# Optimization experiments

Hardware: AMD Instinct MI355X
Metric: run time of the kernel (lower is better)

The kernel has to match this reference:

```python
import jax, jax.numpy as jnp
import numpy as np

DIM = 384
NUM_HEADS = 8
HEAD_DIM = DIM // NUM_HEADS
SCALE = HEAD_DIM ** -0.5
MLP_HIDDEN = int(DIM * 4.0)
EPS = 1e-6


def setup_inputs() -> dict:
    key = jax.random.key(0)
    ks = jax.random.split(key, 8)
    s = 0.02
    return {
        "x": jax.random.normal(ks[0], (2, DIM, 8, 16, 16), dtype=jnp.float32),
        "g1": jnp.ones((DIM,), jnp.float32),
        "b1": jnp.zeros((DIM,), jnp.float32),
        "Wqkv": jax.random.normal(ks[1], (DIM, 3 * DIM), jnp.float32) * s,  # no bias (qkv_bias=False)
        "Wo": jax.random.normal(ks[2], (DIM, DIM), jnp.float32) * s,
        "bo": jnp.zeros((DIM,), jnp.float32),
        "g2": jnp.ones((DIM,), jnp.float32),
        "b2": jnp.zeros((DIM,), jnp.float32),
        "W1": jax.random.normal(ks[3], (DIM, MLP_HIDDEN), jnp.float32) * s,
        "b1m": jnp.zeros((MLP_HIDDEN,), jnp.float32),
        "W2": jax.random.normal(ks[4], (MLP_HIDDEN, DIM), jnp.float32) * s,
        "b2m": jnp.zeros((DIM,), jnp.float32),
    }


def _layernorm(x, g, b):
    mu = jnp.mean(x, axis=-1, keepdims=True)
    var = jnp.mean(jnp.square(x - mu), axis=-1, keepdims=True)
    return (x - mu) * jax.lax.rsqrt(var + EPS) * g + b


def _attention(h, Wqkv, Wo, bo):
    B, N, C = h.shape
    qkv = h @ Wqkv  # [B, N, 3C]
    qkv = qkv.reshape(B, N, 3, NUM_HEADS, HEAD_DIM).transpose(2, 0, 3, 1, 4)
    q, k, v = qkv[0], qkv[1], qkv[2]  # each [B, H, N, d]
    att = jax.nn.softmax(jnp.einsum('bhxd,bhyd->bhxy', q, k) * SCALE, axis=-1)
    out = jnp.einsum('bhxy,bhyd->bhxd', att, v)  # [B, H, N, d]
    out = out.transpose(0, 2, 1, 3).reshape(B, N, C)
    return out @ Wo + bo


def reference(x, g1, b1, Wqkv, Wo, bo, g2, b2, W1, b1m, W2, b2m):
    B, C, D, H, W = x.shape
    h = x.transpose(0, 2, 3, 4, 1).reshape(B, D * H * W, C)  # b (d h w) c
    h = h + _attention(_layernorm(h, g1, b1), Wqkv, Wo, bo)
    m = _layernorm(h, g2, b2)
    m = jax.nn.gelu(m @ W1 + b1m, approximate=False) @ W2 + b2m
    h = h + m
    return h.reshape(B, D, H, W, C).transpose(0, 4, 1, 2, 3)
```

## Files before the change

### kernel.cpp

```cpp
#include <hip/hip_runtime.h>
#include <hip/hip_bf16.h>
#include <math.h>

#define DIM    384
#define NHEAD  8
#define HDIM   48
#define NTOK   2048
#define BATCH  2
#define TOKS   (BATCH * NTOK)
#define HIDDEN 1536

typedef __bf16 bf16x8 __attribute__((ext_vector_type(8)));
typedef float  f32x4  __attribute__((ext_vector_type(4)));
typedef unsigned short u16;

union bfu { __hip_bfloat16 h; u16 u; };

__device__ __forceinline__ void load_lds16(const void* g, void* l) {
    __builtin_amdgcn_global_load_lds(
        (const __attribute__((address_space(1))) void*)g,
        (__attribute__((address_space(3))) void*)l, 16, 0, 0);
}

__global__ __launch_bounds__(256) void prep(
    const float* __restrict__ Wqkv, const float* __restrict__ Wo,
    const float* __restrict__ W1,   const float* __restrict__ W2,
    __hip_bfloat16* __restrict__ WqkvT, __hip_bfloat16* __restrict__ WoT,
    __hip_bfloat16* __restrict__ W1T,   __hip_bfloat16* __restrict__ W2T,
    const float* __restrict__ x, const float* __restrict__ g,
    const float* __restrict__ bta,
    float* __restrict__ hOut, __hip_bfloat16* __restrict__ y) {
    __shared__ __align__(16) char smem[384 * 33 * 4];
    int id = blockIdx.x;
    int tid = threadIdx.x;
    if (id < 1728) {
        float (*t)[33] = (float(*)[33])smem;
        const float* src; __hip_bfloat16* dst; int R, C;
        if (id < 432)       { src = Wqkv; dst = WqkvT; R = 384;  C = 1152; }
        else if (id < 576)  { id -= 432;  src = Wo;    dst = WoT;  R = 384;  C = 384; }
        else if (id < 1152) { id -= 576;  src = W1;    dst = W1T;  R = 384;  C = 1536; }
        else                { id -= 1152; src = W2;    dst = W2T;  R = 1536; C = 384; }
        int tc = C / 32;
        int i0 = (id / tc) * 32, j0 = (id % tc) * 32;
        int tx = tid & 31, ty = tid >> 5;
#pragma unroll
        for (int k = 0; k < 32; k += 8)
            t[ty + k][tx] = src[(size_t)(i0 + ty + k) * C + j0 + tx];
        __syncthreads();
#pragma unroll
        for (int k = 0; k < 32; k += 8)
            dst[(size_t)(j0 + ty + k) * R + i0 + tx] = __float2bfloat16(t[tx][ty + k]);
    } else {
        float* t = (float*)smem;
        int id2 = id - 1728;
        int n0 = (id2 & 63) * 32, b = id2 >> 6;
        const float* xb = x + (size_t)b * DIM * NTOK;
        for (int idx = tid; idx < 384 * 32; idx += 256) {
            int c = idx >> 5, n = idx & 31;
            t[c * 33 + n] = xb[(size_t)c * NTOK + n0 + n];
        }
        __syncthreads();
        int wid = tid >> 6, lane = tid & 63;
#pragma unroll
        for (int it = 0; it < 8; ++it) {
            int tl = it * 4 + wid;
            float v[6];
            float s = 0.f;
#pragma unroll
            for (int i = 0; i < 6; ++i) { v[i] = t[(lane + 64 * i) * 33 + tl]; s += v[i]; }
#pragma unroll
            for (int o = 32; o; o >>= 1) s += __shfl_xor(s, o, 64);
            float mu = s * (1.f / DIM);
            float s2 = 0.f;
#pragma unroll
            for (int i = 0; i < 6; ++i) { float d = v[i] - mu; s2 += d * d; }
#pragma unroll
            for (int o = 32; o; o >>= 1) s2 += __shfl_xor(s2, o, 64);
            float r = rsqrtf(s2 * (1.f / DIM) + 1e-6f);
            size_t tok = (size_t)b * NTOK + n0 + tl;
#pragma unroll
            for (int i = 0; i < 6; ++i) {
                int c = lane + 64 * i;
                hOut[tok * DIM + c] = v[i];
                y[tok * DIM + c] = __float2bfloat16((v[i] - mu) * r * g[c] + bta[c]);
            }
        }
    }
}

template<int BK, bool GELU, bool BF16OUT, bool TRANSOUT, bool QKV>
__global__ __launch_bounds__(256) void gemm_mfma(
    const __hip_bfloat16* __restrict__ A,
    const __hip_bfloat16* __restrict__ BT,
    const float* __restrict__ bias,
    const float* __restrict__ res,
    void* __restrict__ Cout,
    int M, int N, int K,
    __hip_bfloat16* __restrict__ vtout) {
    constexpr int NC = BK / 32;
    __shared__ __align__(16) u16 As[NC][64 * 32];
    __shared__ __align__(16) u16 Bs[NC][64 * 32];
    const int nwg = gridDim.x * gridDim.y;
    const int lid = blockIdx.y * gridDim.x + blockIdx.x;
    const int swz = (lid & 7) * (nwg >> 3) + (lid >> 3);
    const int bx = swz % gridDim.x, by = swz / gridDim.x;
    int bm = by * 64, bn = bx * 64;
    int tid = threadIdx.x;
    int w = tid >> 6, l = tid & 63;
    int m0 = (w >> 1) * 32, n0 = (w & 1) * 32;
    int lm = l & 15, ksel = l >> 4;

    int row = tid >> 2, c16 = tid & 3;
    const __hip_bfloat16* ga = A  + (size_t)(bm + row) * K + c16 * 8;
    const __hip_bfloat16* gb = BT + (size_t)(bn + row) * K + c16 * 8;

    f32x4 acc[2][2] = {};
    for (int k0 = 0; k0 < K; k0 += BK) {
#pragma unroll
        for (int c = 0; c < NC; ++c) {
            load_lds16(ga + k0 + c * 32, &As[c][tid * 8]);
            load_lds16(gb + k0 + c * 32, &Bs[c][tid * 8]);
        }
        __syncthreads();
#pragma unroll
        for (int kk = 0; kk < NC; ++kk) {
            bf16x8 af0 = *(const bf16x8*)&As[kk][(m0 +      lm) * 32 + ksel * 8];
            bf16x8 af1 = *(const bf16x8*)&As[kk][(m0 + 16 + lm) * 32 + ksel * 8];
            bf16x8 bf0 = *(const bf16x8*)&Bs[kk][(n0 +      lm) * 32 + ksel * 8];
            bf16x8 bf1 = *(const bf16x8*)&Bs[kk][(n0 + 16 + lm) * 32 + ksel * 8];
            acc[0][0] = __builtin_amdgcn_mfma_f32_16x16x32_bf16(af0, bf0, acc[0][0], 0, 0, 0);
            acc[0][1] = __builtin_amdgcn_mfma_f32_16x16x32_bf16(af0, bf1, acc[0][1], 0, 0, 0);
            acc[1][0] = __builtin_amdgcn_mfma_f32_16x16x32_bf16(af1, bf0, acc[1][0], 0, 0, 0);
            acc[1][1] = __builtin_amdgcn_mfma_f32_16x16x32_bf16(af1, bf1, acc[1][1], 0, 0, 0);
        }
        __syncthreads();
    }

    if constexpr (TRANSOUT) {
        __shared__ float ct[64 * 65];
#pragma unroll
        for (int i = 0; i < 2; ++i)
#pragma unroll
            for (int j = 0; j < 2; ++j)
#pragma unroll
                for (int r = 0; r < 4; ++r) {
                    int ml = m0 + i * 16 + ksel * 4 + r;
                    int cl = n0 + j * 16 + lm;
                    float v = acc[i][j][r];
                    if (bias) v += bias[bn + cl];
                    if (res)  v += res[(size_t)(bm + ml) * N + bn + cl];
                    ct[ml * 65 + cl] = v;
                }
        __syncthreads();
        int bb = bm >> 11, nb = bm & (NTOK - 1);
        float* outp = (float*)Cout + (size_t)bb * DIM * NTOK + nb;
#pragma unroll
        for (int cl = w; cl < 64; cl += 4)
            outp[(size_t)(bn + cl) * NTOK + l] = ct[l * 65 + cl];
    } else {
#pragma unroll
        for (int i = 0; i < 2; ++i)
#pragma unroll
            for (int j = 0; j < 2; ++j)
#pragma unroll
                for (int r = 0; r < 4; ++r) {
                    int rg = bm + m0 + i * 16 + ksel * 4 + r;
                    int cg = bn + n0 + j * 16 + lm;
                    float v = acc[i][j][r];
                    if (bias) v += bias[cg];
                    if (GELU) v = 0.5f * v * (1.f + erff(v * 0.7071067811865475f));
                    if (res)  v += res[(size_t)rg * N + cg];
                    if constexpr (QKV) {
                        if (cg < 768) {
                            ((__hip_bfloat16*)Cout)[(size_t)rg * 1152 + cg] = __float2bfloat16(v);
                        } else {
                            int c = cg - 768, hh = c / 48, dd = c - hh * 48;
                            int bb = rg >> 11, n = rg & (NTOK - 1);
                            int kk = n & 127;
                            int pos = ((kk >> 6) << 6) + ((kk & 15) << 2) + ((kk >> 4) & 3);
                            vtout[((size_t)(bb * NHEAD + hh) * 48 + dd) * 2048
                                  + (n & ~127) + pos] = __float2bfloat16(v);
                        }
                    } else if constexpr (BF16OUT) {
                        ((__hip_bfloat16*)Cout)[(size_t)rg * N + cg] = __float2bfloat16(v);
                    } else {
                        ((float*)Cout)[(size_t)rg * N + cg] = v;
                    }
                }
    }
}

__global__ __launch_bounds__(256) void wo_ln(
    const __hip_bfloat16* __restrict__ A,
    const __hip_bfloat16* __restrict__ BT,
    const float* __restrict__ bo,
    const float* __restrict__ g2, const float* __restrict__ b2,
    float* __restrict__ h,
    __hip_bfloat16* __restrict__ y) {
    __shared__ __align__(16) u16 As[16 * 64];
    __shared__ __align__(16) u16 Bs[384 * 64];
    __shared__ float red[16 * 8];
    const int r0 = blockIdx.x * 16;
    const int tid = threadIdx.x;
    const int w = tid >> 6, l = tid & 63, lm = l & 15, quad = l >> 4;

    const int arow = tid >> 3;
    const int ag = (tid & 7) ^ (arow & 7);
    const __hip_bfloat16* gaA = A + (size_t)(r0 + arow) * DIM + ag * 8;
    const int xr = lm & 7;

    f32x4 acc[6] = {};
    for (int k0 = 0; k0 < DIM; k0 += 64) {
        if (tid < 128) load_lds16(gaA + k0, (char*)As + tid * 16);
#pragma unroll
        for (int i = 0; i < 12; ++i) {
            int idx = tid + i * 256;
            int brow = idx >> 3;
            int bg = (idx & 7) ^ (brow & 7);
            load_lds16(BT + (size_t)brow * DIM + k0 + bg * 8, (char*)Bs + idx * 16);
        }
        __syncthreads();
#pragma unroll
        for (int kk = 0; kk < 2; ++kk) {
            int goff = ((kk * 4 + quad) ^ xr) * 8;
            bf16x8 af = *(const bf16x8*)&As[lm * 64 + goff];
#pragma unroll
            for (int n = 0; n < 6; ++n) {
                bf16x8 bf = *(const bf16x8*)&Bs[(w * 96 + n * 16 + lm) * 64 + goff];
                acc[n] = __builtin_amdgcn_mfma_f32_16x16x32_bf16(af, bf, acc[n], 0, 0, 0);
            }
        }
        __syncthreads();
    }

    float vv[6][4];
    float s1[4] = {0.f, 0.f, 0.f, 0.f}, s2[4] = {0.f, 0.f, 0.f, 0.f};
#pragma unroll
    for (int r = 0; r < 4; ++r) {
        int rg = r0 + quad * 4 + r;
#pragma unroll
        for (int n = 0; n < 6; ++n) {
            int cg = w * 96 + n * 16 + lm;
            float v = acc[n][r] + bo[cg] + h[(size_t)rg * DIM + cg];
            vv[n][r] = v;
            s1[r] += v;
            s2[r] += v * v;
            h[(size_t)rg * DIM + cg] = v;
        }
    }
#pragma unroll
    for (int r = 0; r < 4; ++r) {
#pragma unroll
        for (int o = 8; o; o >>= 1) {
            s1[r] += __shfl_xor(s1[r], o, 64);
            s2[r] += __shfl_xor(s2[r], o, 64);
        }
        if (lm == 0) {
            red[(quad * 4 + r) * 8 + w * 2]     = s1[r];
            red[(quad * 4 + r) * 8 + w * 2 + 1] = s2[r];
        }
    }
    __syncthreads();
#pragma unroll
    for (int r = 0; r < 4; ++r) {
        int lr = quad * 4 + r;
        float S1 = red[lr * 8] + red[lr * 8 + 2] + red[lr * 8 + 4] + red[lr * 8 + 6];
        float S2 = red[lr * 8 + 1] + red[lr * 8 + 3] + red[lr * 8 + 5] + red[lr * 8 + 7];
        float mu = S1 * (1.f / DIM);
        float var = S2 * (1.f / DIM) - mu * mu;
        float rstd = rsqrtf(var + 1e-6f);
        int rg = r0 + lr;
#pragma unroll
        for (int n = 0; n < 6; ++n) {
            int cg = w * 96 + n * 16 + lm;
            y[(size_t)rg * DIM + cg] =
                __float2bfloat16((vv[n][r] - mu) * rstd * g2[cg] + b2[cg]);
        }
    }
}

#define ATK 128
#define PSTR 136
__global__ __launch_bounds__(512, 4) void attn_mfma(
    const u16* __restrict__ qkv,
    const u16* __restrict__ vt,
    __hip_bfloat16* __restrict__ outp) {
    __shared__ __align__(16) u16 PQ[64 * PSTR];
    __shared__ __align__(16) u16 Ks[128 * 72];
    __shared__ __align__(16) u16 Vs[48 * PSTR];
    const int lid = (blockIdx.z * NHEAD + blockIdx.y) * (NTOK / 64) + blockIdx.x;
    const int swz = (lid & 7) * 64 + (lid >> 3);
    const int q0 = (swz & 31) * 64;
    const int h = (swz >> 5) & 7, b = swz >> 8;
    const int tid = threadIdx.x;
    const int w = tid >> 6, l = tid & 63, lm = l & 15, quad = l >> 4;
    const int qc = w >> 1, kh = w & 1;

    for (int idx = tid; idx < 128; idx += 512) {
        int r = idx >> 1, c = idx & 1;
        *(uint4*)&PQ[r * 72 + 48 + c * 8] = uint4{0, 0, 0, 0};
    }
    for (int idx = tid; idx < 256; idx += 512) {
        int r = idx >> 1, c = idx & 1;
        *(uint4*)&Ks[r * 72 + 48 + c * 8] = uint4{0, 0, 0, 0};
    }
    const u16* qbase = qkv + (size_t)(b * NTOK + q0) * 1152 + h * 48;
    for (int idx = tid; idx < 384; idx += 512) {
        int r = idx / 6, c = idx % 6;
        *(uint4*)&PQ[r * 72 + c * 8] = *(const uint4*)(qbase + (size_t)r * 1152 + c * 8);
    }
    __syncthreads();

    bf16x8 aq0 = *(const bf16x8*)&PQ[(qc * 16 + lm) * 72 +  0 + quad * 8];
    bf16x8 aq1 = *(const bf16x8*)&PQ[(qc * 16 + lm) * 72 + 32 + quad * 8];

    float l_i[4] = {0.f, 0.f, 0.f, 0.f};
    f32x4 o_acc[3] = {};

    const u16* kbase = qkv + (size_t)(b * NTOK) * 1152 + 384 + h * 48;
    const u16* vbase = vt + (size_t)(b * NHEAD + h) * 48 * 2048;
    const float sc2 = 0.14433756729740643f * 1.4426950408889634f;

    const int kr0 = tid / 6,  kc0 = tid % 6;
    const int kr1 = (tid + 512) / 6, kc1 = (tid + 512) % 6;
    const int vd0 = tid >> 4, vc0 = tid & 15;
    const int vd1 = (tid + 512) >> 4, vc1 = (tid + 512) & 15;
    const bool two = tid < 256;
    uint4 kp0, kp1, vp0, vp1;

    {
        kp0 = *(const uint4*)(kbase + (size_t)kr0 * 1152 + kc0 * 8);
        vp0 = *(const uint4*)(vbase + (size_t)vd0 * 2048 + vc0 * 8);
        if (two) {
            kp1 = *(const uint4*)(kbase + (size_t)kr1 * 1152 + kc1 * 8);
            vp1 = *(const uint4*)(vbase + (size_t)vd1 * 2048 + vc1 * 8);
        }
    }

    for (int kt = 0; kt < NTOK / ATK; ++kt) {
        __syncthreads();
        *(uint4*)&Ks[kr0 * 72 + kc0 * 8] = kp0;
        *(uint4*)&Vs[vd0 * PSTR + vc0 * 8] = vp0;
        if (two) {
            *(uint4*)&Ks[kr1 * 72 + kc1 * 8] = kp1;
            *(uint4*)&Vs[vd1 * PSTR + vc1 * 8] = vp1;
        }
        __syncthreads();
        if (kt + 1 < NTOK / ATK) {
            const u16* kb = kbase + (size_t)(kt + 1) * ATK * 1152;
            const u16* vb = vbase + (size_t)(kt + 1) * ATK;
            kp0 = *(const uint4*)(kb + (size_t)kr0 * 1152 + kc0 * 8);
            vp0 = *(const uint4*)(vb + (size_t)vd0 * 2048 + vc0 * 8);
            if (two) {
                kp1 = *(const uint4*)(kb + (size_t)kr1 * 1152 + kc1 * 8);
                vp1 = *(const uint4*)(vb + (size_t)vd1 * 2048 + vc1 * 8);
            }
        }

        f32x4 s[4];
#pragma unroll
        for (int ntp = 0; ntp < 4; ++ntp) {
            int nt = kh * 4 + ntp;
            bf16x8 kf0 = *(const bf16x8*)&Ks[(nt * 16 + lm) * 72 +  0 + quad * 8];
            bf16x8 kf1 = *(const bf16x8*)&Ks[(nt * 16 + lm) * 72 + 32 + quad * 8];
            f32x4 t = {};
            t = __builtin_amdgcn_mfma_f32_16x16x32_bf16(aq0, kf0, t, 0, 0, 0);
            t = __builtin_amdgcn_mfma_f32_16x16x32_bf16(aq1, kf1, t, 0, 0, 0);
            s[ntp] = t;
        }

#pragma unroll
        for (int r = 0; r < 4; ++r) {
            u16 pr[4];
#pragma unroll
            for (int ntp = 0; ntp < 4; ++ntp) {
                float p = exp2f(s[ntp][r] * sc2);
                l_i[r] += p;
                bfu cv; cv.h = __float2bfloat16(p);
                pr[ntp] = cv.u;
            }
            *(uint2*)&PQ[(qc * 16 + quad * 4 + r) * PSTR + kh * 64 + lm * 4] =
                *(const uint2*)pr;
        }

#pragma unroll
        for (int ksp = 0; ksp < 2; ++ksp) {
            int ks = kh * 2 + ksp;
            bf16x8 pf = *(const bf16x8*)&PQ[(qc * 16 + lm) * PSTR + ks * 32 + quad * 8];
#pragma unroll
            for (int nt = 0; nt < 3; ++nt) {
                bf16x8 vf = *(const bf16x8*)&Vs[(nt * 16 + lm) * PSTR + ks * 32 + quad * 8];
                o_acc[nt] = __builtin_amdgcn_mfma_f32_16x16x32_bf16(pf, vf, o_acc[nt], 0, 0, 0);
            }
        }
    }

    __syncthreads();
    float* red = (float*)Ks;
    if (kh == 1) {
        f32x4* base = (f32x4*)&red[(qc * 64 + l) * 16];
        base[0] = o_acc[0]; base[1] = o_acc[1]; base[2] = o_acc[2];
        f32x4 lv; lv[0] = l_i[0]; lv[1] = l_i[1]; lv[2] = l_i[2]; lv[3] = l_i[3];
        base[3] = lv;
    }
    __syncthreads();
    if (kh == 0) {
        f32x4* base = (f32x4*)&red[(qc * 64 + l) * 16];
        o_acc[0] += base[0]; o_acc[1] += base[1]; o_acc[2] += base[2];
        f32x4 lv = base[3];
#pragma unroll
        for (int r = 0; r < 4; ++r) {
            float lsum = l_i[r] + lv[r];
#pragma unroll
            for (int o = 8; o; o >>= 1) lsum += __shfl_xor(lsum, o, 64);
            float inv = 1.f / lsum;
#pragma unroll
            for (int nt = 0; nt < 3; ++nt)
                outp[(size_t)(b * NTOK + q0 + qc * 16 + quad * 4 + r) * DIM
                     + h * 48 + nt * 16 + lm]
                    = __float2bfloat16(o_acc[nt][r] * inv);
        }
    }
}

extern "C" void kernel_launch(void* const* d_in, const int* in_sizes, int n_in,
                              void* d_out, int out_size, void* d_ws, size_t ws_size,
                              hipStream_t stream) {
    const float* x    = (const float*)d_in[0];
    const float* g1   = (const float*)d_in[1];
    const float* b1   = (const float*)d_in[2];
    const float* Wqkv = (const float*)d_in[3];
    const float* Wo   = (const float*)d_in[4];
    const float* bo   = (const float*)d_in[5];
    const float* g2   = (const float*)d_in[6];
    const float* b2   = (const float*)d_in[7];
    const float* W1   = (const float*)d_in[8];
    const float* b1m  = (const float*)d_in[9];
    const float* W2   = (const float*)d_in[10];
    const float* b2m  = (const float*)d_in[11];
    float* out = (float*)d_out;

    char* p = (char*)d_ws;
    float* bufH = (float*)p;                       p += (size_t)TOKS * DIM * 4;
    char* qkvp = p;
    __hip_bfloat16* bufQKVb = (__hip_bfloat16*)p;  p += (size_t)TOKS * 3 * DIM * 2;
    __hip_bfloat16* bufVT   = (__hip_bfloat16*)p;  p += (size_t)TOKS * DIM * 2;
    __hip_bfloat16* bufNb   = (__hip_bfloat16*)p;  p += (size_t)TOKS * DIM * 2;
    __hip_bfloat16* bufAb   = (__hip_bfloat16*)p;  p += (size_t)TOKS * DIM * 2;
    __hip_bfloat16* WqkvT   = (__hip_bfloat16*)p;  p += (size_t)3 * DIM * DIM * 2;
    __hip_bfloat16* WoT     = (__hip_bfloat16*)p;  p += (size_t)DIM * DIM * 2;
    __hip_bfloat16* W1T     = (__hip_bfloat16*)p;  p += (size_t)HIDDEN * DIM * 2;
    __hip_bfloat16* W2T     = (__hip_bfloat16*)p;  p += (size_t)DIM * HIDDEN * 2;
    __hip_bfloat16* bufHIDb = (__hip_bfloat16*)qkvp;

    prep<<<1728 + 128, 256, 0, stream>>>(Wqkv, Wo, W1, W2, WqkvT, WoT, W1T, W2T,
                                         x, g1, b1, bufH, bufNb);
    gemm_mfma<64, false, true, false, true><<<dim3(3 * DIM / 64, TOKS / 64), 256, 0, stream>>>(
        bufNb, WqkvT, nullptr, nullptr, bufQKVb, TOKS, 3 * DIM, DIM, bufVT);
    attn_mfma<<<dim3(NTOK / 64, NHEAD, BATCH), 512, 0, stream>>>(
        (const u16*)bufQKVb, (const u16*)bufVT, bufAb);
    wo_ln<<<TOKS / 16, 256, 0, stream>>>(bufAb, WoT, bo, g2, b2, bufH, bufNb);
    gemm_mfma<64, true, true, false, false><<<dim3(HIDDEN / 64, TOKS / 64), 256, 0, stream>>>(
        bufNb, W1T, b1m, nullptr, bufHIDb, TOKS, HIDDEN, DIM, nullptr);
    gemm_mfma<128, false, false, true, false><<<dim3(DIM / 64, TOKS / 64), 256, 0, stream>>>(
        bufHIDb, W2T, b2m, bufH, out, TOKS, DIM, HIDDEN, nullptr);
}
```

Measured before the change: 187.6 us.

## Double-buffer K/V tiles in LDS and drop zero-padded K stride

Adds a second K and V buffer in shared memory so the next tile is written to the idle buffer after the current tile's MFMAs. This cuts the barriers per key tile from two to one. The K and Q row stride shrinks from 72 to 56, and the upper-quad loads for the second 32-wide head-dim chunk are masked to zero, so the explicit zero-padding writes go away. Shared memory per block rises to roughly 72 KB, which may lower the number of resident blocks per CU.

Result: no change. 189.0 us (+0.8%).

```diff
diff --git a/kernel.cpp b/kernel.cpp
--- a/kernel.cpp
+++ b/kernel.cpp
@@ -281,13 +281,14 @@
 
 #define ATK 128
 #define PSTR 136
+#define KSTR 56
 __global__ __launch_bounds__(512, 4) void attn_mfma(
     const u16* __restrict__ qkv,
     const u16* __restrict__ vt,
     __hip_bfloat16* __restrict__ outp) {
     __shared__ __align__(16) u16 PQ[64 * PSTR];
-    __shared__ __align__(16) u16 Ks[128 * 72];
-    __shared__ __align__(16) u16 Vs[48 * PSTR];
+    __shared__ __align__(16) u16 Ks[2][128 * KSTR];
+    __shared__ __align__(16) u16 Vs[2][48 * PSTR];
     const int lid = (blockIdx.z * NHEAD + blockIdx.y) * (NTOK / 64) + blockIdx.x;
     const int swz = (lid & 7) * 64 + (lid >> 3);
     const int q0 = (swz & 31) * 64;
@@ -296,26 +297,11 @@
     const int w = tid >> 6, l = tid & 63, lm = l & 15, quad = l >> 4;
     const int qc = w >> 1, kh = w & 1;
 
-    for (int idx = tid; idx < 128; idx += 512) {
-        int r = idx >> 1, c = idx & 1;
-        *(uint4*)&PQ[r * 72 + 48 + c * 8] = uint4{0, 0, 0, 0};
-    }
-    for (int idx = tid; idx < 256; idx += 512) {
-        int r = idx >> 1, c = idx & 1;
-        *(uint4*)&Ks[r * 72 + 48 + c * 8] = uint4{0, 0, 0, 0};
-    }
     const u16* qbase = qkv + (size_t)(b * NTOK + q0) * 1152 + h * 48;
     for (int idx = tid; idx < 384; idx += 512) {
         int r = idx / 6, c = idx % 6;
-        *(uint4*)&PQ[r * 72 + c * 8] = *(const uint4*)(qbase + (size_t)r * 1152 + c * 8);
-    }
-    __syncthreads();
-
-    bf16x8 aq0 = *(const bf16x8*)&PQ[(qc * 16 + lm) * 72 +  0 + quad * 8];
-    bf16x8 aq1 = *(const bf16x8*)&PQ[(qc * 16 + lm) * 72 + 32 + quad * 8];
-
-    float l_i[4] = {0.f, 0.f, 0.f, 0.f};
-    f32x4 o_acc[3] = {};
+        *(uint4*)&PQ[r * KSTR + c * 8] = *(const uint4*)(qbase + (size_t)r * 1152 + c * 8);
+    }
 
     const u16* kbase = qkv + (size_t)(b * NTOK) * 1152 + 384 + h * 48;
     const u16* vbase = vt + (size_t)(b * NHEAD + h) * 48 * 2048;
@@ -328,24 +314,30 @@
     const bool two = tid < 256;
     uint4 kp0, kp1, vp0, vp1;
 
-    {
-        kp0 = *(const uint4*)(kbase + (size_t)kr0 * 1152 + kc0 * 8);
-        vp0 = *(const uint4*)(vbase + (size_t)vd0 * 2048 + vc0 * 8);
-        if (two) {
-            kp1 = *(const uint4*)(kbase + (size_t)kr1 * 1152 + kc1 * 8);
-            vp1 = *(const uint4*)(vbase + (size_t)vd1 * 2048 + vc1 * 8);
-        }
-    }
+    kp0 = *(const uint4*)(kbase + (size_t)kr0 * 1152 + kc0 * 8);
+    vp0 = *(const uint4*)(vbase + (size_t)vd0 * 2048 + vc0 * 8);
+    if (two) {
+        kp1 = *(const uint4*)(kbase + (size_t)kr1 * 1152 + kc1 * 8);
+        vp1 = *(const uint4*)(vbase + (size_t)vd1 * 2048 + vc1 * 8);
+    }
+    *(uint4*)&Ks[0][kr0 * KSTR + kc0 * 8] = kp0;
+    *(uint4*)&Vs[0][vd0 * PSTR + vc0 * 8] = vp0;
+    if (two) {
+        *(uint4*)&Ks[0][kr1 * KSTR + kc1 * 8] = kp1;
+        *(uint4*)&Vs[0][vd1 * PSTR + vc1 * 8] = vp1;
+    }
+    __syncthreads();
+
+    bf16x8 aq0 = *(const bf16x8*)&PQ[(qc * 16 + lm) * KSTR + quad * 8];
+    bf16x8 aq1 = {};
+    if (quad < 2) aq1 = *(const bf16x8*)&PQ[(qc * 16 + lm) * KSTR + 32 + quad * 8];
+    __syncthreads();
+
+    float l_i[4] = {0.f, 0.f, 0.f, 0.f};
+    f32x4 o_acc[3] = {};
+    int cur = 0;
 
     for (int kt = 0; kt < NTOK / ATK; ++kt) {
-        __syncthreads();
-        *(uint4*)&Ks[kr0 * 72 + kc0 * 8] = kp0;
-        *(uint4*)&Vs[vd0 * PSTR + vc0 * 8] = vp0;
-        if (two) {
-            *(uint4*)&Ks[kr1 * 72 + kc1 * 8] = kp1;
-            *(uint4*)&Vs[vd1 * PSTR + vc1 * 8] = vp1;
-        }
-        __syncthreads();
         if (kt + 1 < NTOK / ATK) {
             const u16* kb = kbase + (size_t)(kt + 1) * ATK * 1152;
             const u16* vb = vbase + (size_t)(kt + 1) * ATK;
@@ -361,8 +353,10 @@
 #pragma unroll
         for (int ntp = 0; ntp < 4; ++ntp) {
             int nt = kh * 4 + ntp;
-            bf16x8 kf0 = *(const bf16x8*)&Ks[(nt * 16 + lm) * 72 +  0 + quad * 8];
-            bf16x8 kf1 = *(const bf16x8*)&Ks[(nt * 16 + lm) * 72 + 32 + quad * 8];
+            bf16x8 kf0 = *(const bf16x8*)&Ks[cur][(nt * 16 + lm) * KSTR + quad * 8];
+            bf16x8 kf1 = {};
+            if (quad < 2)
+                kf1 = *(const bf16x8*)&Ks[cur][(nt * 16 + lm) * KSTR + 32 + quad * 8];
             f32x4 t = {};
             t = __builtin_amdgcn_mfma_f32_16x16x32_bf16(aq0, kf0, t, 0, 0, 0);
             t = __builtin_amdgcn_mfma_f32_16x16x32_bf16(aq1, kf1, t, 0, 0, 0);
@@ -389,13 +383,23 @@
             bf16x8 pf = *(const bf16x8*)&PQ[(qc * 16 + lm) * PSTR + ks * 32 + quad * 8];
 #pragma unroll
             for (int nt = 0; nt < 3; ++nt) {
-                bf16x8 vf = *(const bf16x8*)&Vs[(nt * 16 + lm) * PSTR + ks * 32 + quad * 8];
+                bf16x8 vf = *(const bf16x8*)&Vs[cur][(nt * 16 + lm) * PSTR + ks * 32 + quad * 8];
                 o_acc[nt] = __builtin_amdgcn_mfma_f32_16x16x32_bf16(pf, vf, o_acc[nt], 0, 0, 0);
             }
         }
-    }
-
-    __syncthreads();
+
+        if (kt + 1 < NTOK / ATK) {
+            *(uint4*)&Ks[cur ^ 1][kr0 * KSTR + kc0 * 8] = kp0;
+            *(uint4*)&Vs[cur ^ 1][vd0 * PSTR + vc0 * 8] = vp0;
+            if (two) {
+                *(uint4*)&Ks[cur ^ 1][kr1 * KSTR + kc1 * 8] = kp1;
+                *(uint4*)&Vs[cur ^ 1][vd1 * PSTR + vc1 * 8] = vp1;
+            }
+        }
+        __syncthreads();
+        cur ^= 1;
+    }
+
     float* red = (float*)Ks;
     if (kh == 1) {
         f32x4* base = (f32x4*)&red[(qc * 64 + l) * 16];
```

## Move Wo/W1/W2 transposes from prep into QKV GEMM launch as extra blocks

Applied to the files above, without the earlier changes.

The prep kernel now transposes only Wqkv plus the LN1 work. The Wo, W1 and W2 transpose-and-cast blocks are appended to a dedicated QKV GEMM kernel, so they run alongside the GEMM tiles instead of delaying the first GEMM. This shortens the critical path before the QKV GEMM, at the cost of a bigger, mixed-workload grid in the second kernel. The weights are still transposed on every call.

Result: no change. 186.4 us (-0.6%).

```diff
diff --git a/kernel.cpp b/kernel.cpp
--- a/kernel.cpp
+++ b/kernel.cpp
@@ -23,36 +23,28 @@
 }
 
 __global__ __launch_bounds__(256) void prep(
-    const float* __restrict__ Wqkv, const float* __restrict__ Wo,
-    const float* __restrict__ W1,   const float* __restrict__ W2,
-    __hip_bfloat16* __restrict__ WqkvT, __hip_bfloat16* __restrict__ WoT,
-    __hip_bfloat16* __restrict__ W1T,   __hip_bfloat16* __restrict__ W2T,
+    const float* __restrict__ Wqkv, __hip_bfloat16* __restrict__ WqkvT,
     const float* __restrict__ x, const float* __restrict__ g,
     const float* __restrict__ bta,
     float* __restrict__ hOut, __hip_bfloat16* __restrict__ y) {
     __shared__ __align__(16) char smem[384 * 33 * 4];
     int id = blockIdx.x;
     int tid = threadIdx.x;
-    if (id < 1728) {
+    if (id < 432) {
         float (*t)[33] = (float(*)[33])smem;
-        const float* src; __hip_bfloat16* dst; int R, C;
-        if (id < 432)       { src = Wqkv; dst = WqkvT; R = 384;  C = 1152; }
-        else if (id < 576)  { id -= 432;  src = Wo;    dst = WoT;  R = 384;  C = 384; }
-        else if (id < 1152) { id -= 576;  src = W1;    dst = W1T;  R = 384;  C = 1536; }
-        else                { id -= 1152; src = W2;    dst = W2T;  R = 1536; C = 384; }
-        int tc = C / 32;
+        const int R = 384, C = 1152, tc = C / 32;
         int i0 = (id / tc) * 32, j0 = (id % tc) * 32;
         int tx = tid & 31, ty = tid >> 5;
 #pragma unroll
         for (int k = 0; k < 32; k += 8)
-            t[ty + k][tx] = src[(size_t)(i0 + ty + k) * C + j0 + tx];
+            t[ty + k][tx] = Wqkv[(size_t)(i0 + ty + k) * C + j0 + tx];
         __syncthreads();
 #pragma unroll
         for (int k = 0; k < 32; k += 8)
-            dst[(size_t)(j0 + ty + k) * R + i0 + tx] = __float2bfloat16(t[tx][ty + k]);
+            WqkvT[(size_t)(j0 + ty + k) * R + i0 + tx] = __float2bfloat16(t[tx][ty + k]);
     } else {
         float* t = (float*)smem;
-        int id2 = id - 1728;
+        int id2 = id - 432;
         int n0 = (id2 & 63) * 32, b = id2 >> 6;
         const float* xb = x + (size_t)b * DIM * NTOK;
         for (int idx = tid; idx < 384 * 32; idx += 256) {
@@ -88,15 +80,101 @@
     }
 }
 
-template<int BK, bool GELU, bool BF16OUT, bool TRANSOUT, bool QKV>
+__global__ __launch_bounds__(256) void qkv_gemm_xpose(
+    const __hip_bfloat16* __restrict__ A,
+    const __hip_bfloat16* __restrict__ BT,
+    __hip_bfloat16* __restrict__ Cout,
+    __hip_bfloat16* __restrict__ vtout,
+    const float* __restrict__ Wo, const float* __restrict__ W1,
+    const float* __restrict__ W2,
+    __hip_bfloat16* __restrict__ WoT, __hip_bfloat16* __restrict__ W1T,
+    __hip_bfloat16* __restrict__ W2T) {
+    __shared__ __align__(16) u16 As[2][64 * 32];
+    __shared__ __align__(16) u16 Bs[2][64 * 32];
+    const int lid = blockIdx.x;
+    const int tid = threadIdx.x;
+    if (lid < 1152) {
+        const int swz = (lid & 7) * 144 + (lid >> 3);
+        const int bx = swz % 18, by = swz / 18;
+        const int bm = by * 64, bn = bx * 64;
+        const int K = DIM;
+        int w = tid >> 6, l = tid & 63;
+        int m0 = (w >> 1) * 32, n0 = (w & 1) * 32;
+        int lm = l & 15, ksel = l >> 4;
+
+        int row = tid >> 2, c16 = tid & 3;
+        const __hip_bfloat16* ga = A  + (size_t)(bm + row) * K + c16 * 8;
+        const __hip_bfloat16* gb = BT + (size_t)(bn + row) * K + c16 * 8;
+
+        f32x4 acc[2][2] = {};
+        for (int k0 = 0; k0 < K; k0 += 64) {
+#pragma unroll
+            for (int c = 0; c < 2; ++c) {
+                load_lds16(ga + k0 + c * 32, &As[c][tid * 8]);
+                load_lds16(gb + k0 + c * 32, &Bs[c][tid * 8]);
+            }
+            __syncthreads();
+#pragma unroll
+            for (int kk = 0; kk < 2; ++kk) {
+                bf16x8 af0 = *(const bf16x8*)&As[kk][(m0 +      lm) * 32 + ksel * 8];
+                bf16x8 af1 = *(const bf16x8*)&As[kk][(m0 + 16 + lm) * 32 + ksel * 8];
+                bf16x8 bf0 = *(const bf16x8*)&Bs[kk][(n0 +      lm) * 32 + ksel * 8];
+                bf16x8 bf1 = *(const bf16x8*)&Bs[kk][(n0 + 16 + lm) * 32 + ksel * 8];
+                acc[0][0] = __builtin_amdgcn_mfma_f32_16x16x32_bf16(af0, bf0, acc[0][0], 0, 0, 0);
+                acc[0][1] = __builtin_amdgcn_mfma_f32_16x16x32_bf16(af0, bf1, acc[0][1], 0, 0, 0);
+                acc[1][0] = __builtin_amdgcn_mfma_f32_16x16x32_bf16(af1, bf0, acc[1][0], 0, 0, 0);
+                acc[1][1] = __builtin_amdgcn_mfma_f32_16x16x32_bf16(af1, bf1, acc[1][1], 0, 0, 0);
+            }
+            __syncthreads();
+        }
+#pragma unroll
+        for (int i = 0; i < 2; ++i)
+#pragma unroll
+            for (int j = 0; j < 2; ++j)
+#pragma unroll
+                for (int r = 0; r < 4; ++r) {
+                    int rg = bm + m0 + i * 16 + ksel * 4 + r;
+                    int cg = bn + n0 + j * 16 + lm;
+                    float v = acc[i][j][r];
+                    if (cg < 768) {
+                        Cout[(size_t)rg * 1152 + cg] = __float2bfloat16(v);
+                    } else {
+                        int c = cg - 768, hh = c / 48, dd = c - hh * 48;
+                        int bb = rg >> 11, n = rg & (NTOK - 1);
+                        int kk = n & 127;
+                        int pos = ((kk >> 6) << 6) + ((kk & 15) << 2) + ((kk >> 4) & 3);
+                        vtout[((size_t)(bb * NHEAD + hh) * 48 + dd) * 2048
+                              + (n & ~127) + pos] = __float2bfloat16(v);
+                    }
+                }
+    } else {
+        float (*t)[33] = (float(*)[33])As;
+        int id = lid - 1152;
+        const float* src; __hip_bfloat16* dst; int R, C;
+        if (id < 144)      {            src = Wo; dst = WoT; R = 384;  C = 384; }
+        else if (id < 720) { id -= 144; src = W1; dst = W1T; R = 384;  C = 1536; }
+        else               { id -= 720; src = W2; dst = W2T; R = 1536; C = 384; }
+        int tc = C / 32;
+        int i0 = (id / tc) * 32, j0 = (id % tc) * 32;
+        int tx = tid & 31, ty = tid >> 5;
+#pragma unroll
+        for (int k = 0; k < 32; k += 8)
+            t[ty + k][tx] = src[(size_t)(i0 + ty + k) * C + j0 + tx];
+        __syncthreads();
+#pragma unroll
+        for (int k = 0; k < 32; k += 8)
+            dst[(size_t)(j0 + ty + k) * R + i0 + tx] = __float2bfloat16(t[tx][ty + k]);
+    }
+}
+
+template<int BK, bool GELU, bool BF16OUT, bool TRANSOUT>
 __global__ __launch_bounds__(256) void gemm_mfma(
     const __hip_bfloat16* __restrict__ A,
     const __hip_bfloat16* __restrict__ BT,
     const float* __restrict__ bias,
     const float* __restrict__ res,
     void* __restrict__ Cout,
-    int M, int N, int K,
-    __hip_bfloat16* __restrict__ vtout) {
+    int M, int N, int K) {
     constexpr int NC = BK / 32;
     __shared__ __align__(16) u16 As[NC][64 * 32];
     __shared__ __align__(16) u16 Bs[NC][64 * 32];
@@ -170,18 +248,7 @@
                     if (bias) v += bias[cg];
                     if (GELU) v = 0.5f * v * (1.f + erff(v * 0.7071067811865475f));
                     if (res)  v += res[(size_t)rg * N + cg];
-                    if constexpr (QKV) {
-                        if (cg < 768) {
-                            ((__hip_bfloat16*)Cout)[(size_t)rg * 1152 + cg] = __float2bfloat16(v);
-                        } else {
-                            int c = cg - 768, hh = c / 48, dd = c - hh * 48;
-                            int bb = rg >> 11, n = rg & (NTOK - 1);
-                            int kk = n & 127;
-                            int pos = ((kk >> 6) << 6) + ((kk & 15) << 2) + ((kk >> 4) & 3);
-                            vtout[((size_t)(bb * NHEAD + hh) * 48 + dd) * 2048
-                                  + (n & ~127) + pos] = __float2bfloat16(v);
-                        }
-                    } else if constexpr (BF16OUT) {
+                    if constexpr (BF16OUT) {
                         ((__hip_bfloat16*)Cout)[(size_t)rg * N + cg] = __float2bfloat16(v);
                     } else {
                         ((float*)Cout)[(size_t)rg * N + cg] = v;
@@ -453,15 +520,14 @@
     __hip_bfloat16* W2T     = (__hip_bfloat16*)p;  p += (size_t)DIM * HIDDEN * 2;
     __hip_bfloat16* bufHIDb = (__hip_bfloat16*)qkvp;
 
-    prep<<<1728 + 128, 256, 0, stream>>>(Wqkv, Wo, W1, W2, WqkvT, WoT, W1T, W2T,
-                                         x, g1, b1, bufH, bufNb);
-    gemm_mfma<64, false, true, false, true><<<dim3(3 * DIM / 64, TOKS / 64), 256, 0, stream>>>(
-        bufNb, WqkvT, nullptr, nullptr, bufQKVb, TOKS, 3 * DIM, DIM, bufVT);
+    prep<<<432 + 128, 256, 0, stream>>>(Wqkv, WqkvT, x, g1, b1, bufH, bufNb);
+    qkv_gemm_xpose<<<1152 + 1296, 256, 0, stream>>>(
+        bufNb, WqkvT, bufQKVb, bufVT, Wo, W1, W2, WoT, W1T, W2T);
     attn_mfma<<<dim3(NTOK / 64, NHEAD, BATCH), 512, 0, stream>>>(
         (const u16*)bufQKVb, (const u16*)bufVT, bufAb);
     wo_ln<<<TOKS / 16, 256, 0, stream>>>(bufAb, WoT, bo, g2, b2, bufH, bufNb);
-    gemm_mfma<64, true, true, false, false><<<dim3(HIDDEN / 64, TOKS / 64), 256, 0, stream>>>(
-        bufNb, W1T, b1m, nullptr, bufHIDb, TOKS, HIDDEN, DIM, nullptr);
-    gemm_mfma<128, false, false, true, false><<<dim3(DIM / 64, TOKS / 64), 256, 0, stream>>>(
-        bufHIDb, W2T, b2m, bufH, out, TOKS, DIM, HIDDEN, nullptr);
-}
+    gemm_mfma<64, true, true, false><<<dim3(HIDDEN / 64, TOKS / 64), 256, 0, stream>>>(
+        bufNb, W1T, b1m, nullptr, bufHIDb, TOKS, HIDDEN, DIM);
+    gemm_mfma<128, false, false, true><<<dim3(DIM / 64, TOKS / 64), 256, 0, stream>>>(
+        bufHIDb, W2T, b2m, bufH, out, TOKS, DIM, HIDDEN);
+}
```
